# Kernel tuning notes

Measured on AMD Instinct MI355X. Metric: run time of the kernel, lower is better.

Reference implementation:

```python
import jax, jax.numpy as jnp
import numpy as np

SCALING = 32.0 / 16.0  # alpha / rank

def setup_inputs() -> dict:
    key = jax.random.key(0)
    k1, k2, k3, k4, k5 = jax.random.split(key, 5)
    B, S, D_IN, D_OUT, R = 4, 2048, 4096, 4096, 16
    x = jax.random.normal(k1, (B, S, D_IN), dtype=jnp.float32)
    weight_int = jax.random.randint(k2, (D_OUT, D_IN), -128, 128, dtype=jnp.int32)
    weight_scale = jax.random.uniform(k3, (1,), dtype=jnp.float32) * 0.01 + 1e-4
    lora_A = jax.random.normal(k4, (R, D_IN), dtype=jnp.float32) * (1.0 / np.sqrt(D_IN))
    lora_B = jax.random.normal(k5, (D_OUT, R), dtype=jnp.float32) * 0.02
    return {"x": x, "weight_int": weight_int, "weight_scale": weight_scale,
            "lora_A": lora_A, "lora_B": lora_B}

def reference(x, weight_int, weight_scale, lora_A, lora_B):
    # Dequantized base weight: [out, in]
    w = weight_int.astype(jnp.float32) * weight_scale  # broadcast scalar scale
    base = jnp.einsum('bsi,oi->bso', x, w)
    # Low-rank LoRA path: (x @ A^T) @ B^T * scaling
    lora = jnp.einsum('bsr,or->bso', jnp.einsum('bsi,ri->bsr', x, lora_A), lora_B) * SCALING
    return base + lora
```

## Files before the change

### kernel.cpp

```cpp
#include <hip/hip_runtime.h>

constexpr int M = 8192;
constexpr int N = 4096;
constexpr int K = 4096;
constexpr float SCALING = 2.0f;

typedef __bf16 bf16x8 __attribute__((ext_vector_type(8)));
typedef __bf16 bf16x4 __attribute__((ext_vector_type(4)));
typedef float  f32x4  __attribute__((ext_vector_type(4)));

__global__ __launch_bounds__(256) void qlora_cast_x(const float* __restrict__ x,
                                                    __bf16* __restrict__ xb) {
    const size_t i = ((size_t)blockIdx.x * 256 + threadIdx.x) * 8;
    const float4 v0 = *(const float4*)(x + i);
    const float4 v1 = *(const float4*)(x + i + 4);
    bf16x8 o;
    o[0] = (__bf16)v0.x; o[1] = (__bf16)v0.y; o[2] = (__bf16)v0.z; o[3] = (__bf16)v0.w;
    o[4] = (__bf16)v1.x; o[5] = (__bf16)v1.y; o[6] = (__bf16)v1.z; o[7] = (__bf16)v1.w;
    *(bf16x8*)(xb + i) = o;
}

__global__ __launch_bounds__(256) void qlora_prep_w(const int* __restrict__ wi,
                                                    const float* __restrict__ wscale,
                                                    const float* __restrict__ lA,
                                                    const float* __restrict__ lB,
                                                    __bf16* __restrict__ W) {
    const int o = blockIdx.x;
    const float s = wscale[0];
    float b[16];
#pragma unroll
    for (int r = 0; r < 16; ++r) b[r] = lB[o * 16 + r];

#pragma unroll
    for (int it = 0; it < 4; ++it) {
        const int i0 = it * 1024 + threadIdx.x * 4;
        const int4 w4 = *(const int4*)(wi + (size_t)o * K + i0);
        float a0 = 0.f, a1 = 0.f, a2 = 0.f, a3 = 0.f;
#pragma unroll
        for (int r = 0; r < 16; ++r) {
            const float4 a4 = *(const float4*)(lA + r * K + i0);
            a0 += b[r] * a4.x; a1 += b[r] * a4.y;
            a2 += b[r] * a4.z; a3 += b[r] * a4.w;
        }
        bf16x4 v;
        v[0] = (__bf16)((float)w4.x * s + SCALING * a0);
        v[1] = (__bf16)((float)w4.y * s + SCALING * a1);
        v[2] = (__bf16)((float)w4.z * s + SCALING * a2);
        v[3] = (__bf16)((float)w4.w * s + SCALING * a3);
        *(bf16x4*)(W + (size_t)o * K + i0) = v;
    }
}

__device__ __forceinline__ void async16(const __bf16* g, __bf16* l) {
    __builtin_amdgcn_global_load_lds(
        (const __attribute__((address_space(1))) unsigned int*)(unsigned long long)g,
        (__attribute__((address_space(3))) unsigned int*)(unsigned int)(unsigned long long)l,
        16, 0, 0);
}

__global__ __launch_bounds__(256) void qlora_gemm_bt(const __bf16* __restrict__ A,
                                                     const __bf16* __restrict__ B,
                                                     float* __restrict__ C) {
    __shared__ __align__(16) __bf16 As[128 * 64];
    __shared__ __align__(16) __bf16 Bs[128 * 64];

    const int tid  = threadIdx.x;
    const int w    = tid >> 6;
    const int lane = tid & 63;
    const int quad = lane >> 4;
    const int lb   = lane & 15;
    const int wm   = w >> 1;
    const int wn   = w & 1;

    const int r8   = lane >> 3;
    const int slot = lane & 7;
    const int q_sw = (slot ^ r8) * 8;

    const size_t mBase = (size_t)blockIdx.y * 128;
    const size_t nBase = (size_t)blockIdx.x * 128;

    const __bf16* gA[4];
    const __bf16* gB[4];
    __bf16* lA[4];
    __bf16* lB[4];
#pragma unroll
    for (int j = 0; j < 4; ++j) {
        const int rt = w * 4 + j;
        gA[j] = A + (mBase + rt * 8 + r8) * K + q_sw;
        gB[j] = B + (nBase + rt * 8 + r8) * K + q_sw;
        lA[j] = As + rt * 512;
        lB[j] = Bs + rt * 512;
    }

    f32x4 acc[4][4] = {};

    for (int kt = 0; kt < K; kt += 64) {
#pragma unroll
        for (int j = 0; j < 4; ++j) async16(gA[j] + kt, lA[j]);
#pragma unroll
        for (int j = 0; j < 4; ++j) async16(gB[j] + kt, lB[j]);
        __syncthreads();

#pragma unroll
        for (int s = 0; s < 2; ++s) {
            bf16x8 af[4], bfr[4];
#pragma unroll
            for (int t = 0; t < 4; ++t) {
                const int rowA = wm * 64 + t * 16 + lb;
                const int rowB = wn * 64 + t * 16 + lb;
                const int sl   = ((s * 4 + quad) ^ (lb & 7)) * 8;
                af[t]  = *(const bf16x8*)(As + rowA * 64 + sl);
                bfr[t] = *(const bf16x8*)(Bs + rowB * 64 + sl);
            }
#pragma unroll
            for (int tm = 0; tm < 4; ++tm)
#pragma unroll
                for (int tn = 0; tn < 4; ++tn)
                    acc[tm][tn] = __builtin_amdgcn_mfma_f32_16x16x32_bf16(
                        af[tm], bfr[tn], acc[tm][tn], 0, 0, 0);
        }
        __syncthreads();
    }

#pragma unroll
    for (int tm = 0; tm < 4; ++tm) {
        const size_t m0 = mBase + wm * 64 + tm * 16 + quad * 4;
#pragma unroll
        for (int tn = 0; tn < 4; ++tn) {
            const size_t n0 = nBase + wn * 64 + tn * 16 + lb;
            float* p = C + m0 * N + n0;
            p[0 * (size_t)N] = acc[tm][tn][0];
            p[1 * (size_t)N] = acc[tm][tn][1];
            p[2 * (size_t)N] = acc[tm][tn][2];
            p[3 * (size_t)N] = acc[tm][tn][3];
        }
    }
}

extern "C" void kernel_launch(void* const* d_in, const int* in_sizes, int n_in,
                              void* d_out, int out_size, void* d_ws, size_t ws_size,
                              hipStream_t stream) {
    const float* x      = (const float*)d_in[0];
    const int*   wint   = (const int*)d_in[1];
    const float* wscale = (const float*)d_in[2];
    const float* lA     = (const float*)d_in[3];
    const float* lB     = (const float*)d_in[4];
    float* out = (float*)d_out;

    __bf16* Xb = (__bf16*)d_ws;
    __bf16* Wb = (__bf16*)((char*)d_ws + (size_t)M * K * 2);

    qlora_cast_x<<<16384, 256, 0, stream>>>(x, Xb);
    qlora_prep_w<<<4096, 256, 0, stream>>>(wint, wscale, lA, lB, Wb);
    qlora_gemm_bt<<<dim3(N / 128, M / 128), 256, 0, stream>>>(Xb, Wb, out);
}
```

Measured before the change: 609.7 us.

## Rewrite GEMM as 256x256 double-buffered 8-wave pipeline; tile LoRA-A in LDS

The main GEMM moves from 128x128 tiles with 4 waves to 256x256 tiles with 8 waves. It double-buffers the LDS tiles (128KB), prefetches the next k-tile while MFMAs run, interleaves fragment loads with MFMA phases using barriers and s_setprio, and swizzles block order to improve L2 reuse. The weight-prep kernel now stages lora_A chunks in shared memory so 16 output rows per block share them, cutting redundant global reads. The costs are heavier register pressure from 32 accumulators per wave, reliance on 2 blocks per CU fitting the LDS budget, and fragile hand-written barrier and waitcnt sequencing.

Measured after the change: 521.7 us. 14.4% less time.

```diff
diff --git a/kernel.cpp b/kernel.cpp
--- a/kernel.cpp
+++ b/kernel.cpp
@@ -25,29 +25,47 @@
                                                     const float* __restrict__ lA,
                                                     const float* __restrict__ lB,
                                                     __bf16* __restrict__ W) {
-    const int o = blockIdx.x;
+    __shared__ __align__(16) float As[16][1028];
+    const int t  = threadIdx.x;
+    const int ol = t >> 4;
+    const int kk = t & 15;
+    const int o  = blockIdx.x * 16 + ol;
     const float s = wscale[0];
     float b[16];
 #pragma unroll
     for (int r = 0; r < 16; ++r) b[r] = lB[o * 16 + r];
 
-#pragma unroll
-    for (int it = 0; it < 4; ++it) {
-        const int i0 = it * 1024 + threadIdx.x * 4;
-        const int4 w4 = *(const int4*)(wi + (size_t)o * K + i0);
-        float a0 = 0.f, a1 = 0.f, a2 = 0.f, a3 = 0.f;
-#pragma unroll
-        for (int r = 0; r < 16; ++r) {
-            const float4 a4 = *(const float4*)(lA + r * K + i0);
-            a0 += b[r] * a4.x; a1 += b[r] * a4.y;
-            a2 += b[r] * a4.z; a3 += b[r] * a4.w;
-        }
-        bf16x4 v;
-        v[0] = (__bf16)((float)w4.x * s + SCALING * a0);
-        v[1] = (__bf16)((float)w4.y * s + SCALING * a1);
-        v[2] = (__bf16)((float)w4.z * s + SCALING * a2);
-        v[3] = (__bf16)((float)w4.w * s + SCALING * a3);
-        *(bf16x4*)(W + (size_t)o * K + i0) = v;
+    for (int c = 0; c < 4; ++c) {
+        const int c0 = c * 1024;
+#pragma unroll
+        for (int i = 0; i < 16; ++i) {
+            const int idx = t + i * 256;
+            const int r   = idx >> 8;
+            const int c4  = idx & 255;
+            const float4 v = *(const float4*)(lA + r * K + c0 + c4 * 4);
+            *(float4*)(&As[r][c4 * 4]) = v;
+        }
+        __syncthreads();
+#pragma unroll
+        for (int j = 0; j < 16; ++j) {
+            const int k4 = kk + j * 16;
+            const int kg = c0 + k4 * 4;
+            const int4 w4 = *(const int4*)(wi + (size_t)o * K + kg);
+            float a0 = 0.f, a1 = 0.f, a2 = 0.f, a3 = 0.f;
+#pragma unroll
+            for (int r = 0; r < 16; ++r) {
+                const float4 a4 = *(const float4*)(&As[r][k4 * 4]);
+                a0 += b[r] * a4.x; a1 += b[r] * a4.y;
+                a2 += b[r] * a4.z; a3 += b[r] * a4.w;
+            }
+            bf16x4 v;
+            v[0] = (__bf16)((float)w4.x * s + SCALING * a0);
+            v[1] = (__bf16)((float)w4.y * s + SCALING * a1);
+            v[2] = (__bf16)((float)w4.z * s + SCALING * a2);
+            v[3] = (__bf16)((float)w4.w * s + SCALING * a3);
+            *(bf16x4*)(W + (size_t)o * K + kg) = v;
+        }
+        __syncthreads();
     }
 }
 
@@ -58,81 +76,152 @@
         16, 0, 0);
 }
 
-__global__ __launch_bounds__(256) void qlora_gemm_bt(const __bf16* __restrict__ A,
-                                                     const __bf16* __restrict__ B,
-                                                     float* __restrict__ C) {
-    __shared__ __align__(16) __bf16 As[128 * 64];
-    __shared__ __align__(16) __bf16 Bs[128 * 64];
+__global__ __launch_bounds__(512, 2) void qlora_gemm_bt(const __bf16* __restrict__ A,
+                                                        const __bf16* __restrict__ B,
+                                                        float* __restrict__ C) {
+    __shared__ __align__(16) __bf16 Lds[65536];
 
     const int tid  = threadIdx.x;
     const int w    = tid >> 6;
     const int lane = tid & 63;
     const int quad = lane >> 4;
     const int lb   = lane & 15;
-    const int wm   = w >> 1;
-    const int wn   = w & 1;
-
-    const int r8   = lane >> 3;
-    const int slot = lane & 7;
-    const int q_sw = (slot ^ r8) * 8;
-
-    const size_t mBase = (size_t)blockIdx.y * 128;
-    const size_t nBase = (size_t)blockIdx.x * 128;
-
-    const __bf16* gA[4];
-    const __bf16* gB[4];
-    __bf16* lA[4];
-    __bf16* lB[4];
-#pragma unroll
-    for (int j = 0; j < 4; ++j) {
-        const int rt = w * 4 + j;
-        gA[j] = A + (mBase + rt * 8 + r8) * K + q_sw;
-        gB[j] = B + (nBase + rt * 8 + r8) * K + q_sw;
-        lA[j] = As + rt * 512;
-        lB[j] = Bs + rt * 512;
+    const int wm   = w >> 2;
+    const int wn   = w & 3;
+
+    const int swz = (blockIdx.x & 7) * 64 + (blockIdx.x >> 3);
+    const int bx  = swz >> 5;
+    const int by  = swz & 31;
+    const size_t mBase = (size_t)by * 256;
+    const size_t nBase = (size_t)bx * 256;
+
+    const int r8 = lane >> 3;
+    const int ch = ((lane & 7) ^ r8) * 8;
+    const __bf16* gA = A + (mBase + w * 32 + r8) * K + ch;
+    const __bf16* gB = B + (nBase + w * 32 + r8) * K + ch;
+    __bf16* lA0 = Lds + w * 2048;
+    __bf16* lB0 = Lds + 16384 + w * 2048;
+
+    const int roA = (wm * 128 + lb) * 64;
+    const int roB = (wn * 64 + lb) * 64;
+    const int sw0 = ((0 + quad) ^ (lb & 7)) * 8;
+    const int sw1 = ((4 + quad) ^ (lb & 7)) * 8;
+
+    f32x4 acc[8][4] = {};
+
+    auto stage = [&](int t) {
+        const int b = t & 1;
+        const size_t kt = (size_t)t * 64;
+        const __bf16* pa = gA + kt;
+        const __bf16* pb = gB + kt;
+        __bf16* la = lA0 + b * 32768;
+        __bf16* lbp = lB0 + b * 32768;
+#pragma unroll
+        for (int j = 0; j < 4; ++j) {
+            async16(pa + (size_t)(j * 8) * K, la + j * 512);
+            async16(pb + (size_t)(j * 8) * K, lbp + j * 512);
+        }
+    };
+
+    auto MF = [](bf16x8 a, bf16x8 b, f32x4 c) {
+        return __builtin_amdgcn_mfma_f32_16x16x32_bf16(a, b, c, 0, 0, 0);
+    };
+
+    stage(0);
+    asm volatile("s_waitcnt vmcnt(0)" ::: "memory");
+    __builtin_amdgcn_s_barrier();
+
+#pragma unroll 2
+    for (int t = 0; t < 64; ++t) {
+        const __bf16* Ab = Lds + (t & 1) * 32768;
+        const __bf16* Bb = Ab + 16384;
+
+        bf16x8 af[4][2], b01[2][2], b23[2][2];
+
+#pragma unroll
+        for (int fm = 0; fm < 4; ++fm) {
+            af[fm][0] = *(const bf16x8*)(Ab + roA + fm * 1024 + sw0);
+            af[fm][1] = *(const bf16x8*)(Ab + roA + fm * 1024 + sw1);
+        }
+#pragma unroll
+        for (int fn = 0; fn < 2; ++fn) {
+            b01[fn][0] = *(const bf16x8*)(Bb + roB + fn * 1024 + sw0);
+            b01[fn][1] = *(const bf16x8*)(Bb + roB + fn * 1024 + sw1);
+        }
+        if (t + 1 < 64) stage(t + 1);
+        __builtin_amdgcn_s_barrier();
+        asm volatile("s_waitcnt lgkmcnt(0)" ::: "memory");
+        __builtin_amdgcn_s_setprio(1);
+#pragma unroll
+        for (int fm = 0; fm < 4; ++fm)
+#pragma unroll
+            for (int fn = 0; fn < 2; ++fn) {
+                acc[fm][fn] = MF(af[fm][0], b01[fn][0], acc[fm][fn]);
+                acc[fm][fn] = MF(af[fm][1], b01[fn][1], acc[fm][fn]);
+            }
+        __builtin_amdgcn_s_setprio(0);
+        __builtin_amdgcn_s_barrier();
+
+#pragma unroll
+        for (int fn = 0; fn < 2; ++fn) {
+            b23[fn][0] = *(const bf16x8*)(Bb + roB + (fn + 2) * 1024 + sw0);
+            b23[fn][1] = *(const bf16x8*)(Bb + roB + (fn + 2) * 1024 + sw1);
+        }
+        __builtin_amdgcn_s_barrier();
+        asm volatile("s_waitcnt lgkmcnt(0)" ::: "memory");
+        __builtin_amdgcn_s_setprio(1);
+#pragma unroll
+        for (int fm = 0; fm < 4; ++fm)
+#pragma unroll
+            for (int fn = 0; fn < 2; ++fn) {
+                acc[fm][fn + 2] = MF(af[fm][0], b23[fn][0], acc[fm][fn + 2]);
+                acc[fm][fn + 2] = MF(af[fm][1], b23[fn][1], acc[fm][fn + 2]);
+            }
+        __builtin_amdgcn_s_setprio(0);
+        __builtin_amdgcn_s_barrier();
+
+#pragma unroll
+        for (int fm = 0; fm < 4; ++fm) {
+            af[fm][0] = *(const bf16x8*)(Ab + roA + (fm + 4) * 1024 + sw0);
+            af[fm][1] = *(const bf16x8*)(Ab + roA + (fm + 4) * 1024 + sw1);
+        }
+        __builtin_amdgcn_s_barrier();
+        asm volatile("s_waitcnt lgkmcnt(0)" ::: "memory");
+        __builtin_amdgcn_s_setprio(1);
+#pragma unroll
+        for (int fm = 0; fm < 4; ++fm)
+#pragma unroll
+            for (int fn = 0; fn < 2; ++fn) {
+                acc[fm + 4][fn] = MF(af[fm][0], b01[fn][0], acc[fm + 4][fn]);
+                acc[fm + 4][fn] = MF(af[fm][1], b01[fn][1], acc[fm + 4][fn]);
+            }
+        __builtin_amdgcn_s_setprio(0);
+        __builtin_amdgcn_s_barrier();
+
+        __builtin_amdgcn_s_setprio(1);
+#pragma unroll
+        for (int fm = 0; fm < 4; ++fm)
+#pragma unroll
+            for (int fn = 0; fn < 2; ++fn) {
+                acc[fm + 4][fn + 2] = MF(af[fm][0], b23[fn][0], acc[fm + 4][fn + 2]);
+                acc[fm + 4][fn + 2] = MF(af[fm][1], b23[fn][1], acc[fm + 4][fn + 2]);
+            }
+        __builtin_amdgcn_s_setprio(0);
+        asm volatile("s_waitcnt vmcnt(0)" ::: "memory");
+        __builtin_amdgcn_s_barrier();
     }
 
-    f32x4 acc[4][4] = {};
-
-    for (int kt = 0; kt < K; kt += 64) {
-#pragma unroll
-        for (int j = 0; j < 4; ++j) async16(gA[j] + kt, lA[j]);
-#pragma unroll
-        for (int j = 0; j < 4; ++j) async16(gB[j] + kt, lB[j]);
-        __syncthreads();
-
-#pragma unroll
-        for (int s = 0; s < 2; ++s) {
-            bf16x8 af[4], bfr[4];
-#pragma unroll
-            for (int t = 0; t < 4; ++t) {
-                const int rowA = wm * 64 + t * 16 + lb;
-                const int rowB = wn * 64 + t * 16 + lb;
-                const int sl   = ((s * 4 + quad) ^ (lb & 7)) * 8;
-                af[t]  = *(const bf16x8*)(As + rowA * 64 + sl);
-                bfr[t] = *(const bf16x8*)(Bs + rowB * 64 + sl);
-            }
-#pragma unroll
-            for (int tm = 0; tm < 4; ++tm)
-#pragma unroll
-                for (int tn = 0; tn < 4; ++tn)
-                    acc[tm][tn] = __builtin_amdgcn_mfma_f32_16x16x32_bf16(
-                        af[tm], bfr[tn], acc[tm][tn], 0, 0, 0);
-        }
-        __syncthreads();
-    }
-
-#pragma unroll
-    for (int tm = 0; tm < 4; ++tm) {
-        const size_t m0 = mBase + wm * 64 + tm * 16 + quad * 4;
-#pragma unroll
-        for (int tn = 0; tn < 4; ++tn) {
-            const size_t n0 = nBase + wn * 64 + tn * 16 + lb;
+#pragma unroll
+    for (int fm = 0; fm < 8; ++fm) {
+        const size_t m0 = mBase + wm * 128 + fm * 16 + quad * 4;
+#pragma unroll
+        for (int fn = 0; fn < 4; ++fn) {
+            const size_t n0 = nBase + wn * 64 + fn * 16 + lb;
             float* p = C + m0 * N + n0;
-            p[0 * (size_t)N] = acc[tm][tn][0];
-            p[1 * (size_t)N] = acc[tm][tn][1];
-            p[2 * (size_t)N] = acc[tm][tn][2];
-            p[3 * (size_t)N] = acc[tm][tn][3];
+            p[0 * (size_t)N] = acc[fm][fn][0];
+            p[1 * (size_t)N] = acc[fm][fn][1];
+            p[2 * (size_t)N] = acc[fm][fn][2];
+            p[3 * (size_t)N] = acc[fm][fn][3];
         }
     }
 }
@@ -151,6 +240,6 @@
     __bf16* Wb = (__bf16*)((char*)d_ws + (size_t)M * K * 2);
 
     qlora_cast_x<<<16384, 256, 0, stream>>>(x, Xb);
-    qlora_prep_w<<<4096, 256, 0, stream>>>(wint, wscale, lA, lB, Wb);
-    qlora_gemm_bt<<<dim3(N / 128, M / 128), 256, 0, stream>>>(Xb, Wb, out);
-}
+    qlora_prep_w<<<256, 256, 0, stream>>>(wint, wscale, lA, lB, Wb);
+    qlora_gemm_bt<<<dim3(512), dim3(512), 0, stream>>>(Xb, Wb, out);
+}
```
